# Kernel tuning notes

Hardware: AMD Instinct MI355X
Metric: run time of the kernel (lower is better)

## Reference

```python
import jax, jax.numpy as jnp
import numpy as np

N_NODES = 20000
N_EDGES = 320000
IN_CH = 256
HID = 128
HEADS = 4
OUT_CH = 16
N_GRAPHS = 128
NEG_SLOPE = 0.2


def setup_inputs() -> dict:
    key = jax.random.key(0)
    ks = jax.random.split(key, 16)
    x = jax.random.normal(ks[0], (N_NODES, IN_CH), dtype=jnp.float32)
    edge_index = jax.random.randint(ks[1], (2, N_EDGES), 0, N_NODES, dtype=jnp.int64)
    batch = jnp.sort(jax.random.randint(ks[2], (N_NODES,), 0, N_GRAPHS, dtype=jnp.int64))
    s = 0.1
    params = {
        # GATConv layer 1: in -> hid, heads=4 (PyG: shared lin for src/dst)
        "W1": jax.random.normal(ks[3], (IN_CH, HEADS * HID), dtype=jnp.float32) * s,
        "as1": jax.random.normal(ks[4], (HEADS, HID), dtype=jnp.float32) * s,
        "ad1": jax.random.normal(ks[5], (HEADS, HID), dtype=jnp.float32) * s,
        "b1": jnp.zeros((HEADS * HID,), dtype=jnp.float32),
        # GATConv layer 2: hid*heads -> hid, heads=1
        "W2": jax.random.normal(ks[6], (HEADS * HID, HID), dtype=jnp.float32) * s,
        "as2": jax.random.normal(ks[7], (1, HID), dtype=jnp.float32) * s,
        "ad2": jax.random.normal(ks[8], (1, HID), dtype=jnp.float32) * s,
        "b2": jnp.zeros((HID,), dtype=jnp.float32),
        # MLP head
        "Wm1": jax.random.normal(ks[9], (HID, HID), dtype=jnp.float32) * s,
        "bm1": jnp.zeros((HID,), dtype=jnp.float32),
        "Wm2": jax.random.normal(ks[10], (HID, OUT_CH), dtype=jnp.float32) * s,
        "bm2": jnp.zeros((OUT_CH,), dtype=jnp.float32),
    }
    return {"x": x, "edge_index": edge_index, "batch": batch, **params}


def _gat_conv(x, W, att_src, att_dst, bias, src, dst, heads, out_ch):
    n = x.shape[0]
    h = (x @ W).reshape(n, heads, out_ch)                 # [N, H, C]
    a_src = jnp.sum(h * att_src, axis=-1)                 # [N, H]
    a_dst = jnp.sum(h * att_dst, axis=-1)                 # [N, H]
    e = jax.nn.leaky_relu(a_src[src] + a_dst[dst], NEG_SLOPE)  # [E, H]
    # segment softmax over edges grouped by destination node
    e_max = jax.ops.segment_max(e, dst, num_segments=n)
    alpha = jnp.exp(e - e_max[dst])
    denom = jax.ops.segment_sum(alpha, dst, num_segments=n)
    alpha = alpha / denom[dst]                            # [E, H]
    msg = h[src] * alpha[..., None]                       # [E, H, C]
    out = jax.ops.segment_sum(msg, dst, num_segments=n)   # [N, H, C]
    return out.reshape(n, heads * out_ch) + bias


def reference(x, edge_index, batch,
              W1, as1, ad1, b1, W2, as2, ad2, b2,
              Wm1, bm1, Wm2, bm2):
    n = x.shape[0]
    loops = jnp.arange(n, dtype=edge_index.dtype)
    src = jnp.concatenate([edge_index[0], loops])         # add self-loops (PyG default)
    dst = jnp.concatenate([edge_index[1], loops])

    h = _gat_conv(x, W1, as1, ad1, b1, src, dst, HEADS, HID)
    h = jax.nn.relu(h)                                    # dropout is identity in eval
    h = _gat_conv(h, W2, as2, ad2, b2, src, dst, 1, HID)

    # global mean pool over graphs
    sums = jax.ops.segment_sum(h, batch, num_segments=N_GRAPHS)
    cnts = jax.ops.segment_sum(jnp.ones((n,), dtype=h.dtype), batch, num_segments=N_GRAPHS)
    pooled = sums / jnp.maximum(cnts, 1.0)[:, None]       # [G, HID]

    # MLP head (dropout identity in eval)
    z = jax.nn.relu(pooled @ Wm1 + bm1)
    return z @ Wm2 + bm2                                  # [G, OUT_CH]
```

## Files before the change

### kernel.cpp

```cpp
#include <hip/hip_runtime.h>
#include <math.h>

#define N_NODES 20000
#define N_EDGES 320000
#define ET (N_EDGES + N_NODES)
#define IN_CH 256
#define HID 128
#define HEADS 4
#define OUT_CH 16
#define N_GRAPHS 128
#define NEG_SLOPE 0.2f
#define LOG2E 1.44269504f

typedef _Float16 f16x8 __attribute__((ext_vector_type(8)));
typedef _Float16 f16x4 __attribute__((ext_vector_type(4)));
typedef _Float16 f16x2 __attribute__((ext_vector_type(2)));
typedef float f32x4 __attribute__((ext_vector_type(4)));
typedef float f32x2 __attribute__((ext_vector_type(2)));

#define LDT 40
__global__ __launch_bounds__(256) void gemm1_f16(const _Float16* __restrict__ A,
    const _Float16* __restrict__ Bt, unsigned char* __restrict__ Cq,
    int M, int N, int K) {
  __shared__ _Float16 As[128 * LDT];
  __shared__ _Float16 Bs[128 * LDT];
  const int bm = blockIdx.y * 128, bn = blockIdx.x * 128;
  const int tid = threadIdx.x;
  const int lane = tid & 63, wv = tid >> 6;
  const int wr = wv >> 1, wc = wv & 1;
  const int r0 = tid >> 2, seg = tid & 3;
  const int m_lo = lane & 15, koff = (lane >> 4) * 8, rq = lane >> 4;
  f32x4 acc[4][4] = {};
  for (int k0 = 0; k0 < K; k0 += 32) {
    const int4 zero4 = {0, 0, 0, 0};
    int gr0 = bm + r0, gr1 = bm + r0 + 64;
    int4 av0 = (gr0 < M) ? *(const int4*)(A + (size_t)gr0 * K + k0 + seg * 8) : zero4;
    int4 av1 = (gr1 < M) ? *(const int4*)(A + (size_t)gr1 * K + k0 + seg * 8) : zero4;
    int4 bv0 = *(const int4*)(Bt + (size_t)(bn + r0) * K + k0 + seg * 8);
    int4 bv1 = *(const int4*)(Bt + (size_t)(bn + r0 + 64) * K + k0 + seg * 8);
    __syncthreads();
    *(int4*)(As + r0 * LDT + seg * 8) = av0;
    *(int4*)(As + (r0 + 64) * LDT + seg * 8) = av1;
    *(int4*)(Bs + r0 * LDT + seg * 8) = bv0;
    *(int4*)(Bs + (r0 + 64) * LDT + seg * 8) = bv1;
    __syncthreads();
    f16x8 af[4], bf[4];
    #pragma unroll
    for (int i = 0; i < 4; i++)
      af[i] = *(const f16x8*)(As + (wr * 64 + i * 16 + m_lo) * LDT + koff);
    #pragma unroll
    for (int j = 0; j < 4; j++)
      bf[j] = *(const f16x8*)(Bs + (wc * 64 + j * 16 + m_lo) * LDT + koff);
    #pragma unroll
    for (int i = 0; i < 4; i++)
      #pragma unroll
      for (int j = 0; j < 4; j++)
        acc[i][j] = __builtin_amdgcn_mfma_f32_16x16x32_f16(af[i], bf[j], acc[i][j], 0, 0, 0);
  }
  #pragma unroll
  for (int i = 0; i < 4; i++)
    #pragma unroll
    for (int r = 0; r < 4; r++) {
      int grow = bm + wr * 64 + i * 16 + rq * 4 + r;
      if (grow < M)
        #pragma unroll
        for (int j = 0; j < 4; j++) {
          int gcol = bn + wc * 64 + j * 16 + m_lo;
          float v = acc[i][j][r];
          Cq[(size_t)grow * N + gcol] =
              (unsigned char)(__builtin_amdgcn_cvt_pk_fp8_f32(v, v, 0, false) & 0xFF);
        }
    }
}

__global__ __launch_bounds__(256) void gemm2_f16(const _Float16* __restrict__ A,
    const _Float16* __restrict__ Bt, _Float16* __restrict__ C,
    int M, int N, int K) {
  __shared__ _Float16 As[128 * LDT];
  __shared__ _Float16 Bs[64 * LDT];
  const int bm = blockIdx.y * 128, bn = blockIdx.x * 64;
  const int tid = threadIdx.x;
  const int lane = tid & 63, wv = tid >> 6;
  const int ra = tid >> 1, sa = (tid & 1) * 16;
  const int rb = tid >> 2, sb = (tid & 3) * 8;
  const int m_lo = lane & 15, koff = (lane >> 4) * 8, rq = lane >> 4;
  f32x4 acc[2][4] = {};
  for (int k0 = 0; k0 < K; k0 += 32) {
    const int4 zero4 = {0, 0, 0, 0};
    int gra = bm + ra;
    int4 a0 = (gra < M) ? *(const int4*)(A + (size_t)gra * K + k0 + sa) : zero4;
    int4 a1 = (gra < M) ? *(const int4*)(A + (size_t)gra * K + k0 + sa + 8) : zero4;
    int4 b0 = *(const int4*)(Bt + (size_t)(bn + rb) * K + k0 + sb);
    __syncthreads();
    *(int4*)(As + ra * LDT + sa) = a0;
    *(int4*)(As + ra * LDT + sa + 8) = a1;
    *(int4*)(Bs + rb * LDT + sb) = b0;
    __syncthreads();
    f16x8 af[2], bf[4];
    #pragma unroll
    for (int i = 0; i < 2; i++)
      af[i] = *(const f16x8*)(As + (wv * 32 + i * 16 + m_lo) * LDT + koff);
    #pragma unroll
    for (int j = 0; j < 4; j++)
      bf[j] = *(const f16x8*)(Bs + (j * 16 + m_lo) * LDT + koff);
    #pragma unroll
    for (int i = 0; i < 2; i++)
      #pragma unroll
      for (int j = 0; j < 4; j++)
        acc[i][j] = __builtin_amdgcn_mfma_f32_16x16x32_f16(af[i], bf[j], acc[i][j], 0, 0, 0);
  }
  #pragma unroll
  for (int i = 0; i < 2; i++)
    #pragma unroll
    for (int r = 0; r < 4; r++) {
      int grow = bm + wv * 32 + i * 16 + rq * 4 + r;
      if (grow < M)
        #pragma unroll
        for (int j = 0; j < 4; j++) {
          int gcol = bn + j * 16 + m_lo;
          C[(size_t)grow * N + gcol] = (_Float16)acc[i][j][r];
        }
    }
}

#define S0 N_NODES
#define S1 (IN_CH * HEADS * HID)
#define S2 (HEADS * HID * HID)
#define S3 (8 * IN_CH)
#define S4 (HEADS * HID)
#define S5 (N_GRAPHS + 1)
#define PREP_TOTAL (S0 + S1 + S2 + S3 + S4 + S5)
__global__ void prep_kernel(const float* __restrict__ W1, const float* __restrict__ W2,
    const float* __restrict__ as1, const float* __restrict__ ad1,
    const float* __restrict__ as2, const float* __restrict__ ad2,
    const int* __restrict__ batch, int* __restrict__ cnt,
    _Float16* __restrict__ W1T, _Float16* __restrict__ W2T,
    float* __restrict__ wt1, float* __restrict__ wt2, int* __restrict__ goff) {
  int idx = blockIdx.x * blockDim.x + threadIdx.x;
  if (idx < S0) { cnt[idx] = 0; return; }
  idx -= S0;
  if (idx < S1) {
    int n = idx >> 8, k = idx & 255;
    W1T[idx] = (_Float16)W1[(size_t)k * (HEADS * HID) + n];
    return;
  }
  idx -= S1;
  if (idx < S2) {
    int n = idx >> 9, k = idx & 511;
    W2T[idx] = (_Float16)W2[(size_t)k * HID + n];
    return;
  }
  idx -= S2;
  if (idx < S3) {
    int j = idx >> 8, i = idx & 255;
    int sd = j >> 2, h = j & 3;
    const float* av = sd ? ad1 : as1;
    float s = 0.f;
    for (int c = 0; c < HID; ++c)
      s += W1[(size_t)i * (HEADS * HID) + h * HID + c] * av[h * HID + c];
    wt1[idx] = s * LOG2E;
    return;
  }
  idx -= S3;
  if (idx < S4) {
    float s = 0.f, d = 0.f;
    for (int j = 0; j < HID; ++j) {
      float w = W2[(size_t)idx * HID + j];
      s += w * as2[j];
      d += w * ad2[j];
    }
    wt2[idx] = s * LOG2E;
    wt2[HEADS * HID + idx] = d * LOG2E;
    return;
  }
  idx -= S4;
  if (idx < S5) {
    int g = idx;
    int lo = 0, hi = N_NODES;
    while (lo < hi) {
      int mid = (lo + hi) >> 1;
      if (batch[mid] < g) lo = mid + 1; else hi = mid;
    }
    goff[g] = lo;
  }
}

__global__ __launch_bounds__(256) void conv_x(const float* __restrict__ x,
    const float* __restrict__ wt1, _Float16* __restrict__ xb,
    float* __restrict__ a1s, float* __restrict__ a1d) {
  int node = blockIdx.x * 4 + (threadIdx.x >> 6);
  int lane = threadIdx.x & 63;
  if (node >= N_NODES) return;
  int c = lane * 4;
  float4 xv = *(const float4*)(x + (size_t)node * IN_CH + c);
  *(f16x4*)(xb + (size_t)node * IN_CH + c) =
      f16x4{(_Float16)xv.x, (_Float16)xv.y, (_Float16)xv.z, (_Float16)xv.w};
  float p[8];
  #pragma unroll
  for (int jj = 0; jj < 8; ++jj) {
    float4 w = *(const float4*)(wt1 + jj * IN_CH + c);
    p[jj] = xv.x * w.x + xv.y * w.y + xv.z * w.z + xv.w * w.w;
  }
  #pragma unroll
  for (int o = 32; o > 0; o >>= 1)
    #pragma unroll
    for (int jj = 0; jj < 8; ++jj) p[jj] += __shfl_down(p[jj], o);
  if (lane == 0) {
    #pragma unroll
    for (int h = 0; h < 4; ++h) {
      a1s[node * HEADS + h] = p[h];
      a1d[node * HEADS + h] = p[4 + h];
    }
  }
}

__global__ void hist_kernel(const int* __restrict__ dst, int* __restrict__ cnt) {
  int i = blockIdx.x * blockDim.x + threadIdx.x;
  if (i >= ET) return;
  int d = (i < N_EDGES) ? dst[i] : (i - N_EDGES);
  atomicAdd(&cnt[d], 1);
}

#define SCH 20
__global__ __launch_bounds__(1024) void scan_kernel(const int* __restrict__ cnt,
    int* __restrict__ offs, int* __restrict__ cursor, int n) {
  int tid = threadIdx.x;
  int base = tid * SCH;
  int v[SCH];
  int s = 0;
  #pragma unroll
  for (int i = 0; i < SCH; i++) {
    int idx = base + i;
    int t = (idx < n) ? cnt[idx] : 0;
    v[i] = s; s += t;
  }
  int lane = tid & 63, wv = tid >> 6;
  int x = s;
  #pragma unroll
  for (int o = 1; o < 64; o <<= 1) {
    int t = __shfl_up(x, o);
    if (lane >= o) x += t;
  }
  __shared__ int wsum[16];
  if (lane == 63) wsum[wv] = x;
  __syncthreads();
  if (tid == 0) {
    int r = 0;
    for (int w = 0; w < 16; w++) { int t = wsum[w]; wsum[w] = r; r += t; }
  }
  __syncthreads();
  int excl = x - s + wsum[wv];
  #pragma unroll
  for (int i = 0; i < SCH; i++) {
    int idx = base + i;
    if (idx < n) { offs[idx] = excl + v[i]; cursor[idx] = excl + v[i]; }
  }
  if (tid == 1023) offs[n] = excl + s;
}

__global__ void fill_kernel(const int* __restrict__ src, const int* __restrict__ dst,
                            int* __restrict__ cursor, int* __restrict__ csr) {
  int e = blockIdx.x * blockDim.x + threadIdx.x;
  if (e >= ET) return;
  int s, d;
  if (e < N_EDGES) { s = src[e]; d = dst[e]; } else { s = d = e - N_EDGES; }
  int pos = atomicAdd(&cursor[d], 1);
  csr[pos] = s;
}

__global__ __launch_bounds__(256) void agg1_kernel(
    const unsigned char* __restrict__ h1q, const float* __restrict__ a1s,
    const float* __restrict__ a1d, const int* __restrict__ offs,
    const int* __restrict__ csr, const float* __restrict__ b1,
    const float* __restrict__ wt2, _Float16* __restrict__ h1rb,
    float* __restrict__ a2s, float* __restrict__ a2d) {
  int wv = threadIdx.x >> 6, lane = threadIdx.x & 63;
  int n = blockIdx.x * 4 + wv;
  int c0 = lane * 8;
  int h = lane >> 4;
  float ad_n = a1d[n * HEADS + h];
  int e0 = offs[n], e1 = offs[n + 1];
  float acc[8] = {};
  float den = 0.f;
  for (int e = e0; e < e1; e += 8) {
    int s[8]; float av[8]; uint2 q[8];
    #pragma unroll
    for (int j = 0; j < 8; j++) {
      int ee = e + j;
      s[j] = csr[(ee < e1) ? ee : e1 - 1];
    }
    #pragma unroll
    for (int j = 0; j < 8; j++) {
      av[j] = ((e + j) < e1) ? a1s[s[j] * HEADS + h] : -16384.f;
      q[j] = *(const uint2*)(h1q + (size_t)s[j] * (HEADS * HID) + c0);
    }
    #pragma unroll
    for (int j = 0; j < 8; j++) {
      float aa = av[j] + ad_n;
      aa = (aa > 0.f) ? aa : NEG_SLOPE * aa;
      float al = exp2f(aa);
      f32x2 p0 = __builtin_amdgcn_cvt_pk_f32_fp8(q[j].x, false);
      f32x2 p1 = __builtin_amdgcn_cvt_pk_f32_fp8(q[j].x, true);
      f32x2 p2 = __builtin_amdgcn_cvt_pk_f32_fp8(q[j].y, false);
      f32x2 p3 = __builtin_amdgcn_cvt_pk_f32_fp8(q[j].y, true);
      acc[0] += al * p0.x; acc[1] += al * p0.y;
      acc[2] += al * p1.x; acc[3] += al * p1.y;
      acc[4] += al * p2.x; acc[5] += al * p2.y;
      acc[6] += al * p3.x; acc[7] += al * p3.y;
      den += al;
    }
  }
  float inv = 1.f / den;
  f16x8 ov;
  float ps = 0.f, pd = 0.f;
  #pragma unroll
  for (int i = 0; i < 8; i++) {
    float o = fmaxf(acc[i] * inv + b1[c0 + i], 0.f);
    ov[i] = (_Float16)o;
    ps += o * wt2[c0 + i];
    pd += o * wt2[HEADS * HID + c0 + i];
  }
  *(f16x8*)(h1rb + (size_t)n * (HEADS * HID) + c0) = ov;
  #pragma unroll
  for (int o = 32; o > 0; o >>= 1) { ps += __shfl_down(ps, o); pd += __shfl_down(pd, o); }
  if (lane == 0) { a2s[n] = ps; a2d[n] = pd; }
}

__global__ __launch_bounds__(256) void agg2_kernel(
    const _Float16* __restrict__ h2b, const float* __restrict__ a2s,
    const float* __restrict__ a2d, const int* __restrict__ offs,
    const int* __restrict__ csr, const float* __restrict__ b2,
    float* __restrict__ h2a) {
  int wv = threadIdx.x >> 6, lane = threadIdx.x & 63;
  int n = blockIdx.x * 4 + wv;
  int c = lane * 2;
  float ad_n = a2d[n];
  int e0 = offs[n], e1 = offs[n + 1];
  float acc0 = 0.f, acc1 = 0.f, den = 0.f;
  for (int e = e0; e < e1; e += 8) {
    int s[8]; float av[8]; f16x2 q[8];
    #pragma unroll
    for (int j = 0; j < 8; j++) {
      int ee = e + j;
      s[j] = csr[(ee < e1) ? ee : e1 - 1];
    }
    #pragma unroll
    for (int j = 0; j < 8; j++) {
      av[j] = ((e + j) < e1) ? a2s[s[j]] : -16384.f;
      q[j] = *(const f16x2*)(h2b + (size_t)s[j] * HID + c);
    }
    #pragma unroll
    for (int j = 0; j < 8; j++) {
      float aa = av[j] + ad_n;
      aa = (aa > 0.f) ? aa : NEG_SLOPE * aa;
      float al = exp2f(aa);
      acc0 += al * (float)q[j].x;
      acc1 += al * (float)q[j].y;
      den += al;
    }
  }
  float inv = 1.f / den;
  *(float2*)&h2a[(size_t)n * HID + c] =
      make_float2(acc0 * inv + b2[c], acc1 * inv + b2[c + 1]);
}

__global__ __launch_bounds__(256) void pool_mlp(const float* __restrict__ h2a,
    const int* __restrict__ goff, const float* __restrict__ Wm1,
    const float* __restrict__ bm1, const float* __restrict__ Wm2,
    const float* __restrict__ bm2, float* __restrict__ outp) {
  __shared__ float part[2][HID];
  __shared__ float pl[HID];
  __shared__ float z[HID];
  int g = blockIdx.x, tid = threadIdx.x;
  int c = tid & 127, half = tid >> 7;
  int n0 = goff[g], n1 = goff[g + 1];
  float acc = 0.f;
  for (int n = n0 + half; n < n1; n += 2)
    acc += h2a[(size_t)n * HID + c];
  part[half][c] = acc;
  __syncthreads();
  if (tid < HID) {
    float inv = 1.f / fmaxf((float)(n1 - n0), 1.f);
    pl[tid] = (part[0][tid] + part[1][tid]) * inv;
  }
  __syncthreads();
  if (tid < HID) {
    float s = bm1[tid];
    for (int k = 0; k < HID; ++k) s += pl[k] * Wm1[k * HID + tid];
    z[tid] = fmaxf(s, 0.f);
  }
  __syncthreads();
  if (tid < OUT_CH) {
    float o = bm2[tid];
    for (int k = 0; k < HID; ++k) o += z[k] * Wm2[k * OUT_CH + tid];
    outp[g * OUT_CH + tid] = o;
  }
}

extern "C" void kernel_launch(void* const* d_in, const int* in_sizes, int n_in,
                              void* d_out, int out_size, void* d_ws, size_t ws_size,
                              hipStream_t stream) {
  const float* x    = (const float*)d_in[0];
  const int*   ei   = (const int*)d_in[1];
  const int*   batch= (const int*)d_in[2];
  const float* W1   = (const float*)d_in[3];
  const float* as1  = (const float*)d_in[4];
  const float* ad1  = (const float*)d_in[5];
  const float* b1   = (const float*)d_in[6];
  const float* W2   = (const float*)d_in[7];
  const float* as2  = (const float*)d_in[8];
  const float* ad2  = (const float*)d_in[9];
  const float* b2   = (const float*)d_in[10];
  const float* Wm1  = (const float*)d_in[11];
  const float* bm1  = (const float*)d_in[12];
  const float* Wm2  = (const float*)d_in[13];
  const float* bm2  = (const float*)d_in[14];
  float* outp = (float*)d_out;
  const int* srcp = ei;
  const int* dstp = ei + N_EDGES;

  char* p = (char*)d_ws;
  auto alloc = [&](size_t bytes) {
    char* r = p; p += (bytes + 255) & ~(size_t)255; return r;
  };
  _Float16* xb   = (_Float16*)alloc((size_t)N_NODES * IN_CH * 2);
  unsigned char* h1q = (unsigned char*)alloc((size_t)N_NODES * HEADS * HID);
  _Float16* h1rb = (_Float16*)alloc((size_t)N_NODES * HEADS * HID * 2);
  _Float16* h2b  = (_Float16*)alloc((size_t)N_NODES * HID * 2);
  float*    h2a  = (float*)alloc((size_t)N_NODES * HID * 4);
  _Float16* W1T  = (_Float16*)alloc((size_t)(HEADS * HID) * IN_CH * 2);
  _Float16* W2T  = (_Float16*)alloc((size_t)HID * (HEADS * HID) * 2);
  float* wt1     = (float*)alloc(8 * IN_CH * 4);
  float* wt2     = (float*)alloc(2 * (HEADS * HID) * 4);
  float* a1s     = (float*)alloc((size_t)N_NODES * HEADS * 4);
  float* a1d     = (float*)alloc((size_t)N_NODES * HEADS * 4);
  float* a2s     = (float*)alloc((size_t)N_NODES * 4);
  float* a2d     = (float*)alloc((size_t)N_NODES * 4);
  int*   cnt     = (int*)alloc((size_t)N_NODES * 4);
  int*   offs    = (int*)alloc((size_t)(N_NODES + 1) * 4);
  int*   cursor  = (int*)alloc((size_t)N_NODES * 4);
  int*   csr     = (int*)alloc((size_t)ET * 4);
  int*   goff    = (int*)alloc((size_t)(N_GRAPHS + 1) * 4);

  prep_kernel<<<(PREP_TOTAL + 255) / 256, 256, 0, stream>>>(
      W1, W2, as1, ad1, as2, ad2, batch, cnt, W1T, W2T, wt1, wt2, goff);

  conv_x<<<(N_NODES + 3) / 4, 256, 0, stream>>>(x, wt1, xb, a1s, a1d);

  hist_kernel<<<(ET + 255) / 256, 256, 0, stream>>>(dstp, cnt);
  scan_kernel<<<1, 1024, 0, stream>>>(cnt, offs, cursor, N_NODES);
  fill_kernel<<<(ET + 255) / 256, 256, 0, stream>>>(srcp, dstp, cursor, csr);

  gemm1_f16<<<dim3((HEADS * HID) / 128, (N_NODES + 127) / 128), 256, 0, stream>>>(
      xb, W1T, h1q, N_NODES, HEADS * HID, IN_CH);

  agg1_kernel<<<N_NODES / 4, 256, 0, stream>>>(
      h1q, a1s, a1d, offs, csr, b1, wt2, h1rb, a2s, a2d);

  gemm2_f16<<<dim3(HID / 64, (N_NODES + 127) / 128), 256, 0, stream>>>(
      h1rb, W2T, h2b, N_NODES, HID, HEADS * HID);

  agg2_kernel<<<N_NODES / 4, 256, 0, stream>>>(h2b, a2s, a2d, offs, csr, b2, h2a);

  pool_mlp<<<N_GRAPHS, 256, 0, stream>>>(h2a, goff, Wm1, bm1, Wm2, bm2, outp);
}
```

Measured before the change: 274.1 us.

## Fuse preprocessing, histogram, scan and CSR fill into co-scheduled kernels

Merges independent stages into shared launches to cut kernel count. The weight prep now also does the degree histogram, and counter zeroing moves to a memset. The 1024-thread scan becomes an extra block inside the x-conversion kernel, now using 256 threads with 80 elements each, and the CSR fill shares a launch with the first GEMM as extra blocks. This removes several launch gaps and serial dependencies, but the single scan block now does more serial work per thread and may finish later than the conversion blocks.

```diff
diff --git a/kernel.cpp b/kernel.cpp
--- a/kernel.cpp
+++ b/kernel.cpp
@@ -19,12 +19,154 @@
 typedef float f32x2 __attribute__((ext_vector_type(2)));
 
 #define LDT 40
-__global__ __launch_bounds__(256) void gemm1_f16(const _Float16* __restrict__ A,
+
+#define P1 (IN_CH * HEADS * HID)
+#define P2 (HEADS * HID * HID)
+#define P3 (8 * IN_CH)
+#define P4 (HEADS * HID)
+#define P5 (N_GRAPHS + 1)
+#define P6 ET
+#define PH_TOTAL (P1 + P2 + P3 + P4 + P5 + P6)
+__global__ void prep_hist(const float* __restrict__ W1, const float* __restrict__ W2,
+    const float* __restrict__ as1, const float* __restrict__ ad1,
+    const float* __restrict__ as2, const float* __restrict__ ad2,
+    const int* __restrict__ batch, const int* __restrict__ dst,
+    int* __restrict__ cnt,
+    _Float16* __restrict__ W1T, _Float16* __restrict__ W2T,
+    float* __restrict__ wt1, float* __restrict__ wt2, int* __restrict__ goff) {
+  int idx = blockIdx.x * blockDim.x + threadIdx.x;
+  if (idx < P1) {
+    int n = idx >> 8, k = idx & 255;
+    W1T[idx] = (_Float16)W1[(size_t)k * (HEADS * HID) + n];
+    return;
+  }
+  idx -= P1;
+  if (idx < P2) {
+    int n = idx >> 9, k = idx & 511;
+    W2T[idx] = (_Float16)W2[(size_t)k * HID + n];
+    return;
+  }
+  idx -= P2;
+  if (idx < P3) {
+    int j = idx >> 8, i = idx & 255;
+    int sd = j >> 2, h = j & 3;
+    const float* av = sd ? ad1 : as1;
+    float s = 0.f;
+    for (int c = 0; c < HID; ++c)
+      s += W1[(size_t)i * (HEADS * HID) + h * HID + c] * av[h * HID + c];
+    wt1[idx] = s * LOG2E;
+    return;
+  }
+  idx -= P3;
+  if (idx < P4) {
+    float s = 0.f, d = 0.f;
+    for (int j = 0; j < HID; ++j) {
+      float w = W2[(size_t)idx * HID + j];
+      s += w * as2[j];
+      d += w * ad2[j];
+    }
+    wt2[idx] = s * LOG2E;
+    wt2[HEADS * HID + idx] = d * LOG2E;
+    return;
+  }
+  idx -= P4;
+  if (idx < P5) {
+    int g = idx;
+    int lo = 0, hi = N_NODES;
+    while (lo < hi) {
+      int mid = (lo + hi) >> 1;
+      if (batch[mid] < g) lo = mid + 1; else hi = mid;
+    }
+    goff[g] = lo;
+    return;
+  }
+  idx -= P5;
+  if (idx < P6) {
+    int d = (idx < N_EDGES) ? dst[idx] : (idx - N_EDGES);
+    atomicAdd(&cnt[d], 1);
+  }
+}
+
+#define SCB 5000
+__global__ __launch_bounds__(256) void conv_scan(const float* __restrict__ x,
+    const float* __restrict__ wt1, _Float16* __restrict__ xb,
+    float* __restrict__ a1s, float* __restrict__ a1d,
+    const int* __restrict__ cnt, int* __restrict__ offs, int* __restrict__ cursor) {
+  __shared__ int wsum[4];
+  if (blockIdx.x == SCB) {
+    int tid = threadIdx.x;
+    int base = tid * 80;
+    int s = 0;
+    for (int i = 0; i < 80; i++) {
+      int idx = base + i;
+      if (idx < N_NODES) s += cnt[idx];
+    }
+    int lane = tid & 63, w = tid >> 6;
+    int xv = s;
+    #pragma unroll
+    for (int o = 1; o < 64; o <<= 1) {
+      int t = __shfl_up(xv, o);
+      if (lane >= o) xv += t;
+    }
+    if (lane == 63) wsum[w] = xv;
+    __syncthreads();
+    int carry = 0;
+    for (int i = 0; i < w; i++) carry += wsum[i];
+    int run = carry + xv - s;
+    for (int i = 0; i < 80; i++) {
+      int idx = base + i;
+      if (idx < N_NODES) { offs[idx] = run; cursor[idx] = run; run += cnt[idx]; }
+    }
+    if (tid == 255) offs[N_NODES] = run;
+    return;
+  }
+  int node = blockIdx.x * 4 + (threadIdx.x >> 6);
+  int lane = threadIdx.x & 63;
+  if (node >= N_NODES) return;
+  int c = lane * 4;
+  float4 xv = *(const float4*)(x + (size_t)node * IN_CH + c);
+  *(f16x4*)(xb + (size_t)node * IN_CH + c) =
+      f16x4{(_Float16)xv.x, (_Float16)xv.y, (_Float16)xv.z, (_Float16)xv.w};
+  float p[8];
+  #pragma unroll
+  for (int jj = 0; jj < 8; ++jj) {
+    float4 w = *(const float4*)(wt1 + jj * IN_CH + c);
+    p[jj] = xv.x * w.x + xv.y * w.y + xv.z * w.z + xv.w * w.w;
+  }
+  #pragma unroll
+  for (int o = 32; o > 0; o >>= 1)
+    #pragma unroll
+    for (int jj = 0; jj < 8; ++jj) p[jj] += __shfl_down(p[jj], o);
+  if (lane == 0) {
+    #pragma unroll
+    for (int h = 0; h < 4; ++h) {
+      a1s[node * HEADS + h] = p[h];
+      a1d[node * HEADS + h] = p[4 + h];
+    }
+  }
+}
+
+#define FILL_BLOCKS ((ET + 255) / 256)
+#define G1_BN ((HEADS * HID) / 128)
+#define G1_BM ((N_NODES + 127) / 128)
+__global__ __launch_bounds__(256) void gemm1_fill(const _Float16* __restrict__ A,
     const _Float16* __restrict__ Bt, unsigned char* __restrict__ Cq,
-    int M, int N, int K) {
+    const int* __restrict__ src, const int* __restrict__ dst,
+    int* __restrict__ cursor, int* __restrict__ csr) {
   __shared__ _Float16 As[128 * LDT];
   __shared__ _Float16 Bs[128 * LDT];
-  const int bm = blockIdx.y * 128, bn = blockIdx.x * 128;
+  if (blockIdx.x < FILL_BLOCKS) {
+    int e = blockIdx.x * 256 + threadIdx.x;
+    if (e >= ET) return;
+    int s, d;
+    if (e < N_EDGES) { s = src[e]; d = dst[e]; } else { s = d = e - N_EDGES; }
+    int pos = atomicAdd(&cursor[d], 1);
+    csr[pos] = s;
+    return;
+  }
+  const int g = blockIdx.x - FILL_BLOCKS;
+  const int bm = (g >> 2) * 128, bn = (g & 3) * 128;
+  const int M = N_NODES, N = HEADS * HID, K = IN_CH;
   const int tid = threadIdx.x;
   const int lane = tid & 63, wv = tid >> 6;
   const int wr = wv >> 1, wc = wv & 1;
@@ -123,151 +265,6 @@
     }
 }
 
-#define S0 N_NODES
-#define S1 (IN_CH * HEADS * HID)
-#define S2 (HEADS * HID * HID)
-#define S3 (8 * IN_CH)
-#define S4 (HEADS * HID)
-#define S5 (N_GRAPHS + 1)
-#define PREP_TOTAL (S0 + S1 + S2 + S3 + S4 + S5)
-__global__ void prep_kernel(const float* __restrict__ W1, const float* __restrict__ W2,
-    const float* __restrict__ as1, const float* __restrict__ ad1,
-    const float* __restrict__ as2, const float* __restrict__ ad2,
-    const int* __restrict__ batch, int* __restrict__ cnt,
-    _Float16* __restrict__ W1T, _Float16* __restrict__ W2T,
-    float* __restrict__ wt1, float* __restrict__ wt2, int* __restrict__ goff) {
-  int idx = blockIdx.x * blockDim.x + threadIdx.x;
-  if (idx < S0) { cnt[idx] = 0; return; }
-  idx -= S0;
-  if (idx < S1) {
-    int n = idx >> 8, k = idx & 255;
-    W1T[idx] = (_Float16)W1[(size_t)k * (HEADS * HID) + n];
-    return;
-  }
-  idx -= S1;
-  if (idx < S2) {
-    int n = idx >> 9, k = idx & 511;
-    W2T[idx] = (_Float16)W2[(size_t)k * HID + n];
-    return;
-  }
-  idx -= S2;
-  if (idx < S3) {
-    int j = idx >> 8, i = idx & 255;
-    int sd = j >> 2, h = j & 3;
-    const float* av = sd ? ad1 : as1;
-    float s = 0.f;
-    for (int c = 0; c < HID; ++c)
-      s += W1[(size_t)i * (HEADS * HID) + h * HID + c] * av[h * HID + c];
-    wt1[idx] = s * LOG2E;
-    return;
-  }
-  idx -= S3;
-  if (idx < S4) {
-    float s = 0.f, d = 0.f;
-    for (int j = 0; j < HID; ++j) {
-      float w = W2[(size_t)idx * HID + j];
-      s += w * as2[j];
-      d += w * ad2[j];
-    }
-    wt2[idx] = s * LOG2E;
-    wt2[HEADS * HID + idx] = d * LOG2E;
-    return;
-  }
-  idx -= S4;
-  if (idx < S5) {
-    int g = idx;
-    int lo = 0, hi = N_NODES;
-    while (lo < hi) {
-      int mid = (lo + hi) >> 1;
-      if (batch[mid] < g) lo = mid + 1; else hi = mid;
-    }
-    goff[g] = lo;
-  }
-}
-
-__global__ __launch_bounds__(256) void conv_x(const float* __restrict__ x,
-    const float* __restrict__ wt1, _Float16* __restrict__ xb,
-    float* __restrict__ a1s, float* __restrict__ a1d) {
-  int node = blockIdx.x * 4 + (threadIdx.x >> 6);
-  int lane = threadIdx.x & 63;
-  if (node >= N_NODES) return;
-  int c = lane * 4;
-  float4 xv = *(const float4*)(x + (size_t)node * IN_CH + c);
-  *(f16x4*)(xb + (size_t)node * IN_CH + c) =
-      f16x4{(_Float16)xv.x, (_Float16)xv.y, (_Float16)xv.z, (_Float16)xv.w};
-  float p[8];
-  #pragma unroll
-  for (int jj = 0; jj < 8; ++jj) {
-    float4 w = *(const float4*)(wt1 + jj * IN_CH + c);
-    p[jj] = xv.x * w.x + xv.y * w.y + xv.z * w.z + xv.w * w.w;
-  }
-  #pragma unroll
-  for (int o = 32; o > 0; o >>= 1)
-    #pragma unroll
-    for (int jj = 0; jj < 8; ++jj) p[jj] += __shfl_down(p[jj], o);
-  if (lane == 0) {
-    #pragma unroll
-    for (int h = 0; h < 4; ++h) {
-      a1s[node * HEADS + h] = p[h];
-      a1d[node * HEADS + h] = p[4 + h];
-    }
-  }
-}
-
-__global__ void hist_kernel(const int* __restrict__ dst, int* __restrict__ cnt) {
-  int i = blockIdx.x * blockDim.x + threadIdx.x;
-  if (i >= ET) return;
-  int d = (i < N_EDGES) ? dst[i] : (i - N_EDGES);
-  atomicAdd(&cnt[d], 1);
-}
-
-#define SCH 20
-__global__ __launch_bounds__(1024) void scan_kernel(const int* __restrict__ cnt,
-    int* __restrict__ offs, int* __restrict__ cursor, int n) {
-  int tid = threadIdx.x;
-  int base = tid * SCH;
-  int v[SCH];
-  int s = 0;
-  #pragma unroll
-  for (int i = 0; i < SCH; i++) {
-    int idx = base + i;
-    int t = (idx < n) ? cnt[idx] : 0;
-    v[i] = s; s += t;
-  }
-  int lane = tid & 63, wv = tid >> 6;
-  int x = s;
-  #pragma unroll
-  for (int o = 1; o < 64; o <<= 1) {
-    int t = __shfl_up(x, o);
-    if (lane >= o) x += t;
-  }
-  __shared__ int wsum[16];
-  if (lane == 63) wsum[wv] = x;
-  __syncthreads();
-  if (tid == 0) {
-    int r = 0;
-    for (int w = 0; w < 16; w++) { int t = wsum[w]; wsum[w] = r; r += t; }
-  }
-  __syncthreads();
-  int excl = x - s + wsum[wv];
-  #pragma unroll
-  for (int i = 0; i < SCH; i++) {
-    int idx = base + i;
-    if (idx < n) { offs[idx] = excl + v[i]; cursor[idx] = excl + v[i]; }
-  }
-  if (tid == 1023) offs[n] = excl + s;
-}
-
-__global__ void fill_kernel(const int* __restrict__ src, const int* __restrict__ dst,
-                            int* __restrict__ cursor, int* __restrict__ csr) {
-  int e = blockIdx.x * blockDim.x + threadIdx.x;
-  if (e >= ET) return;
-  int s, d;
-  if (e < N_EDGES) { s = src[e]; d = dst[e]; } else { s = d = e - N_EDGES; }
-  int pos = atomicAdd(&cursor[d], 1);
-  csr[pos] = s;
-}
-
 __global__ __launch_bounds__(256) void agg1_kernel(
     const unsigned char* __restrict__ h1q, const float* __restrict__ a1s,
     const float* __restrict__ a1d, const int* __restrict__ offs,
@@ -442,17 +439,15 @@
   int*   csr     = (int*)alloc((size_t)ET * 4);
   int*   goff    = (int*)alloc((size_t)(N_GRAPHS + 1) * 4);
 
-  prep_kernel<<<(PREP_TOTAL + 255) / 256, 256, 0, stream>>>(
-      W1, W2, as1, ad1, as2, ad2, batch, cnt, W1T, W2T, wt1, wt2, goff);
-
-  conv_x<<<(N_NODES + 3) / 4, 256, 0, stream>>>(x, wt1, xb, a1s, a1d);
-
-  hist_kernel<<<(ET + 255) / 256, 256, 0, stream>>>(dstp, cnt);
-  scan_kernel<<<1, 1024, 0, stream>>>(cnt, offs, cursor, N_NODES);
-  fill_kernel<<<(ET + 255) / 256, 256, 0, stream>>>(srcp, dstp, cursor, csr);
-
-  gemm1_f16<<<dim3((HEADS * HID) / 128, (N_NODES + 127) / 128), 256, 0, stream>>>(
-      xb, W1T, h1q, N_NODES, HEADS * HID, IN_CH);
+  hipMemsetAsync(cnt, 0, (size_t)N_NODES * 4, stream);
+
+  prep_hist<<<(PH_TOTAL + 255) / 256, 256, 0, stream>>>(
+      W1, W2, as1, ad1, as2, ad2, batch, dstp, cnt, W1T, W2T, wt1, wt2, goff);
+
+  conv_scan<<<SCB + 1, 256, 0, stream>>>(x, wt1, xb, a1s, a1d, cnt, offs, cursor);
+
+  gemm1_fill<<<FILL_BLOCKS + G1_BN * G1_BM, 256, 0, stream>>>(
+      xb, W1T, h1q, srcp, dstp, cursor, csr);
 
   agg1_kernel<<<N_NODES / 4, 256, 0, stream>>>(
       h1q, a1s, a1d, offs, csr, b1, wt2, h1rb, a2s, a2d);
```

New measurement: 293.2 us. 1.07x slower.
